# Optimization experiments

Hardware: AMD Instinct MI355X
Metric: run time of the kernel (lower is better)

Reference implementation:

```python
import jax, jax.numpy as jnp
import numpy as np

B, S, D = 4, 2048, 1024
H = 16
DH = D // H  # dim_q = dim_k = 64
F = 4096
EPS = 1e-5


def setup_inputs() -> dict:
    key = jax.random.key(0)
    ks = jax.random.split(key, 16)
    sd = 0.02
    inp = {
        'x': jax.random.normal(ks[0], (B, S, D), jnp.float32),
        'wq': jax.random.normal(ks[1], (H, D, DH), jnp.float32) * sd,
        'bq': jnp.zeros((H, DH), jnp.float32),
        'wk': jax.random.normal(ks[2], (H, D, DH), jnp.float32) * sd,
        'bk': jnp.zeros((H, DH), jnp.float32),
        'wv': jax.random.normal(ks[3], (H, D, DH), jnp.float32) * sd,
        'bv': jnp.zeros((H, DH), jnp.float32),
        'wo': jax.random.normal(ks[4], (H * DH, D), jnp.float32) * sd,
        'bo': jnp.zeros((D,), jnp.float32),
        'ln1_g': jnp.ones((D,), jnp.float32),
        'ln1_b': jnp.zeros((D,), jnp.float32),
        'w1': jax.random.normal(ks[5], (D, F), jnp.float32) * sd,
        'b1': jnp.zeros((F,), jnp.float32),
        'w2': jax.random.normal(ks[6], (F, D), jnp.float32) * sd,
        'b2': jnp.zeros((D,), jnp.float32),
        'ln2_g': jnp.ones((D,), jnp.float32),
        'ln2_b': jnp.zeros((D,), jnp.float32),
    }
    return inp


def _layernorm(x, g, b):
    mu = jnp.mean(x, axis=-1, keepdims=True)
    var = jnp.mean(jnp.square(x - mu), axis=-1, keepdims=True)
    return (x - mu) * jax.lax.rsqrt(var + EPS) * g + b


def _encoder_layer(x, wq, bq, wk, bk, wv, bv, wo, bo, ln1_g, ln1_b,
                   w1, b1, w2, b2, ln2_g, ln2_b):
    # Multi-head attention (all heads batched via einsum)
    q = jnp.einsum('bsd,hde->bhse', x, wq) + bq[:, None, :]
    k = jnp.einsum('bsd,hde->bhse', x, wk) + bk[:, None, :]
    v = jnp.einsum('bsd,hde->bhse', x, wv) + bv[:, None, :]
    scores = jnp.einsum('bhqe,bhke->bhqk', q, k) / jnp.sqrt(jnp.float32(DH))
    p = jax.nn.softmax(scores, axis=-1)
    o = jnp.einsum('bhqk,bhke->bhqe', p, v)  # [B,H,S,DH]
    o = o.transpose(0, 2, 1, 3).reshape(B, S, H * DH)  # concat heads
    attn = o @ wo + bo
    y = _layernorm(x + attn, ln1_g, ln1_b)  # post-norm residual
    # Feed-forward
    ff = jax.nn.relu(y @ w1 + b1) @ w2 + b2
    return _layernorm(y + ff, ln2_g, ln2_b)


def reference(x, wq, bq, wk, bk, wv, bv, wo, bo, ln1_g, ln1_b,
              w1, b1, w2, b2, ln2_g, ln2_b):
    return _encoder_layer(x, wq, bq, wk, bk, wv, bv, wo, bo, ln1_g, ln1_b,
                          w1, b1, w2, b2, ln2_g, ln2_b)
```

## Files before the change

kernel.cpp:

```cpp
#include <hip/hip_runtime.h>
#include <stdint.h>


typedef short bf16x8 __attribute__((ext_vector_type(8)));
typedef unsigned short u16x8 __attribute__((ext_vector_type(8)));
typedef float f32x4 __attribute__((ext_vector_type(4)));
typedef unsigned int u32x2 __attribute__((ext_vector_type(2)));

#define MFMA16(a, b, c) __builtin_amdgcn_mfma_f32_16x16x32_bf16((a), (b), (c), 0, 0, 0)

#define QSCALE 0.1803368801111204f

__device__ __forceinline__ float b2f(unsigned short u) {
    union { unsigned u32; float f; } x;
    x.u32 = ((unsigned)u) << 16;
    return x.f;
}
__device__ __forceinline__ unsigned short f2b(float f) {
    union { float f; unsigned u; } x;
    x.f = f;
    unsigned r = x.u + 0x7fff + ((x.u >> 16) & 1);
    return (unsigned short)(r >> 16);
}

__device__ __forceinline__ void gl16(const unsigned short* g, unsigned short* l) {
    __builtin_amdgcn_global_load_lds(
        (__attribute__((address_space(1))) unsigned int*)(unsigned long)g,
        (__attribute__((address_space(3))) unsigned int*)l, 16, 0, 0);
}

__global__ __launch_bounds__(256) void f2b_bulk(const float* __restrict__ in,
                                                unsigned short* __restrict__ out) {
    const long i = ((long)blockIdx.x * 256 + threadIdx.x) * 8;
    float4 a = *(const float4*)&in[i];
    float4 b = *(const float4*)&in[i + 4];
    u16x8 u;
    u[0] = f2b(a.x); u[1] = f2b(a.y); u[2] = f2b(a.z); u[3] = f2b(a.w);
    u[4] = f2b(b.x); u[5] = f2b(b.y); u[6] = f2b(b.z); u[7] = f2b(b.w);
    *(u16x8*)&out[i] = u;
}

__global__ void transpose_f2b(const float* __restrict__ in,
                              unsigned short* __restrict__ out,
                              int R, int C, long in_batch_stride,
                              int out_row0, int out_ld) {
    __shared__ float tile[32][33];
    const int batch = blockIdx.z;
    const float* src = in + (long)batch * in_batch_stride;
    const int c0 = blockIdx.x * 32, r0 = blockIdx.y * 32;
    const int tx = threadIdx.x, ty = threadIdx.y;
#pragma unroll
    for (int i = 0; i < 32; i += 8)
        tile[ty + i][tx] = src[(long)(r0 + ty + i) * C + c0 + tx];
    __syncthreads();
#pragma unroll
    for (int i = 0; i < 32; i += 8)
        out[(long)(out_row0 + batch * C + c0 + ty + i) * out_ld + r0 + tx] =
            f2b(tile[tx][ty + i]);
}

__global__ void transpose_v(const unsigned short* __restrict__ qkv,
                            unsigned short* __restrict__ vt) {
    __shared__ unsigned short tile[32][33];
    const int bh = blockIdx.z;
    const int b = bh >> 4, h = bh & 15;
    const int s0 = blockIdx.x * 32, e0 = blockIdx.y * 32;
    const int tx = threadIdx.x, ty = threadIdx.y;
    const unsigned short* src = qkv + ((long)b * 2048) * 3072 + 2048 + h * 64;
#pragma unroll
    for (int i = 0; i < 32; i += 8)
        tile[ty + i][tx] = src[(long)(s0 + ty + i) * 3072 + e0 + tx];
    __syncthreads();
    unsigned short* dst = vt + ((long)bh * 64) * 2048;
#pragma unroll
    for (int i = 0; i < 32; i += 8)
        dst[(long)(e0 + ty + i) * 2048 + s0 + tx] = tile[tx][ty + i];
}

__global__ void concat_bias(const float* __restrict__ bq,
                            const float* __restrict__ bk,
                            const float* __restrict__ bv,
                            float* __restrict__ out) {
    int n = blockIdx.x * 256 + threadIdx.x;
    out[n] = (n < 1024) ? bq[n] : (n < 2048) ? bk[n - 1024] : bv[n - 2048];
}

__device__ __forceinline__ float to_f(float v) { return v; }
__device__ __forceinline__ float to_f(unsigned short v) { return b2f(v); }

template <typename RT>
__global__ __launch_bounds__(512, 2) void gemm256(
    const unsigned short* __restrict__ A, const unsigned short* __restrict__ Bt,
    unsigned short* __restrict__ C, const float* __restrict__ bias,
    const RT* __restrict__ resid, int M, int N, int K, int op) {
    __shared__ __align__(16) unsigned short As[4][256 * 32];
    __shared__ __align__(16) unsigned short Bs[4][256 * 32];
    const int tid = threadIdx.x;
    const int lane = tid & 63;
    const int wave = tid >> 6;
    const int quad = lane >> 4, lr = lane & 15;
    const int wr = wave >> 2, wc = wave & 3;

    const int nx = gridDim.x;
    const int nwg = nx * gridDim.y;
    const int orig = blockIdx.y * nx + blockIdx.x;
    const int wg = (orig & 7) * (nwg >> 3) + (orig >> 3);
    const long n0 = (long)(wg % nx) * 256;
    const long m0 = (long)(wg / nx) * 256;

    f32x4 acc[8][4] = {};

    const int trow = tid >> 2;
    const int tch = ((tid & 3) ^ ((tid >> 3) & 3)) * 8;
    const unsigned short* gA0 = A + (m0 + trow) * (long)K + tch;
    const unsigned short* gA1 = A + (m0 + 128 + trow) * (long)K + tch;
    const unsigned short* gB0 = Bt + (n0 + trow) * (long)K + tch;
    const unsigned short* gB1 = Bt + (n0 + 128 + trow) * (long)K + tch;
    unsigned short* const dA = &As[0][0] + tid * 8;
    unsigned short* const dB = &Bs[0][0] + tid * 8;

    int aoff[8], boff[4];
#pragma unroll
    for (int mi = 0; mi < 8; mi++) {
        const int r = wr * 128 + mi * 16 + lr;
        aoff[mi] = r * 32 + (quad ^ ((r >> 1) & 3)) * 8;
    }
#pragma unroll
    for (int ni = 0; ni < 4; ni++) {
        const int r = wc * 64 + ni * 16 + lr;
        boff[ni] = r * 32 + (quad ^ ((r >> 1) & 3)) * 8;
    }

#define STAGE_A(si)                                                   \
    {                                                                 \
        gl16(gA0 + (long)(si) * 32, dA + ((si) & 3) * 8192);          \
        gl16(gA1 + (long)(si) * 32, dA + ((si) & 3) * 8192 + 4096);   \
    }
#define STAGE_B(si)                                                   \
    {                                                                 \
        gl16(gB0 + (long)(si) * 32, dB + ((si) & 3) * 8192);          \
        gl16(gB1 + (long)(si) * 32, dB + ((si) & 3) * 8192 + 4096);   \
    }

    const int S = K >> 5;
    for (int s = 0; s < 3; s++) {
        STAGE_A(s);
        STAGE_B(s);
    }
    asm volatile("s_waitcnt vmcnt(8)" ::: "memory");
    __builtin_amdgcn_s_barrier();

    for (int s = 0; s < S; ++s) {
        const int slot = s & 3;
        const unsigned short* as_ = &As[slot][0];
        const unsigned short* bs_ = &Bs[slot][0];
        const bool st = (s + 3) < S;
        bf16x8 af[8], bf[4];
#pragma unroll
        for (int mi = 0; mi < 8; mi++) af[mi] = *(const bf16x8*)&as_[aoff[mi]];
        bf[0] = *(const bf16x8*)&bs_[boff[0]];
        bf[1] = *(const bf16x8*)&bs_[boff[1]];
        if (st) STAGE_A(s + 3);
        __builtin_amdgcn_s_barrier();
        asm volatile("s_waitcnt lgkmcnt(0)" ::: "memory");
        __builtin_amdgcn_sched_barrier(0);
        __builtin_amdgcn_s_setprio(1);
#pragma unroll
        for (int mi = 0; mi < 8; mi++) {
            acc[mi][0] = MFMA16(af[mi], bf[0], acc[mi][0]);
            acc[mi][1] = MFMA16(af[mi], bf[1], acc[mi][1]);
        }
        __builtin_amdgcn_s_setprio(0);
        __builtin_amdgcn_s_barrier();
        __builtin_amdgcn_sched_barrier(0);
        bf[2] = *(const bf16x8*)&bs_[boff[2]];
        bf[3] = *(const bf16x8*)&bs_[boff[3]];
        if (st) STAGE_B(s + 3);
        __builtin_amdgcn_s_barrier();
        asm volatile("s_waitcnt lgkmcnt(0)" ::: "memory");
        __builtin_amdgcn_sched_barrier(0);
        __builtin_amdgcn_s_setprio(1);
#pragma unroll
        for (int mi = 0; mi < 8; mi++) {
            acc[mi][2] = MFMA16(af[mi], bf[2], acc[mi][2]);
            acc[mi][3] = MFMA16(af[mi], bf[3], acc[mi][3]);
        }
        __builtin_amdgcn_s_setprio(0);
        if (s + 3 < S) {
            asm volatile("s_waitcnt vmcnt(8)" ::: "memory");
        } else if (s + 2 < S) {
            asm volatile("s_waitcnt vmcnt(4)" ::: "memory");
        } else {
            asm volatile("s_waitcnt vmcnt(0)" ::: "memory");
        }
        __builtin_amdgcn_s_barrier();
        __builtin_amdgcn_sched_barrier(0);
    }
#undef STAGE_A
#undef STAGE_B

#pragma unroll
    for (int ni = 0; ni < 4; ni++) {
        const long col = n0 + wc * 64 + ni * 16 + lr;
        const float bv = bias ? bias[col] : 0.0f;
        const float cscale = (op == 2 && col < 1024) ? QSCALE : 1.0f;
#pragma unroll
        for (int mi = 0; mi < 8; mi++) {
#pragma unroll
            for (int r = 0; r < 4; r++) {
                const long row = m0 + wr * 128 + mi * 16 + quad * 4 + r;
                float v = (acc[mi][ni][r] + bv) * cscale;
                if (resid) v += to_f(resid[row * (long)N + col]);
                if (op == 1) v = fmaxf(v, 0.0f);
                C[row * (long)N + col] = f2b(v);
            }
        }
    }
}

template <int TAG, typename RT>
__global__ __launch_bounds__(512, 2) void gemmK64(
    const unsigned short* __restrict__ A, const unsigned short* __restrict__ Bt,
    unsigned short* __restrict__ C, const float* __restrict__ bias,
    const RT* __restrict__ resid, int M, int N, int K, int op) {
    __shared__ __align__(16) unsigned short As[3][256 * 64];
    __shared__ __align__(16) unsigned short Bs[3][128 * 64];
    const int tid = threadIdx.x;
    const int lane = tid & 63;
    const int wave = tid >> 6;
    const int quad = lane >> 4, lr = lane & 15;
    const int wr = wave >> 1, wc = wave & 1;

    const int nx = gridDim.x;
    const int nwg = nx * gridDim.y;
    const int orig = blockIdx.y * nx + blockIdx.x;
    const int wg = (orig & 7) * (nwg >> 3) + (orig >> 3);
    const long n0 = (long)(wg % nx) * 128;
    const long m0 = (long)(wg / nx) * 256;

    f32x4 acc[4][4] = {};

    const int trow = tid >> 3;
    const int tch = ((tid & 7) ^ ((tid >> 4) & 7)) * 8;
    const unsigned short* gA = A + (m0 + trow) * (long)K + tch;
    const unsigned short* gB = Bt + (n0 + trow) * (long)K + tch;
    const long rs64 = 64 * (long)K;
    unsigned short* const dA = &As[0][0] + tid * 8;
    unsigned short* const dB = &Bs[0][0] + tid * 8;

    int aoff[2][4], boff[2][4];
#pragma unroll
    for (int kc = 0; kc < 2; kc++) {
#pragma unroll
        for (int mi = 0; mi < 4; mi++) {
            const int r = wr * 64 + mi * 16 + lr;
            aoff[kc][mi] = r * 64 + (((kc << 2) | quad) ^ ((r >> 1) & 7)) * 8;
        }
#pragma unroll
        for (int ni = 0; ni < 4; ni++) {
            const int r = wc * 64 + ni * 16 + lr;
            boff[kc][ni] = r * 64 + (((kc << 2) | quad) ^ ((r >> 1) & 7)) * 8;
        }
    }

#define KSTAGE_H1(si)                                                   \
    {                                                                   \
        const long _kk = (long)(si) * 64;                               \
        const int _sl = (si) % 3;                                       \
        gl16(gA + _kk, dA + _sl * 16384);                               \
        gl16(gA + rs64 + _kk, dA + _sl * 16384 + 4096);                 \
        gl16(gB + _kk, dB + _sl * 8192);                                \
    }
#define KSTAGE_H2(si)                                                   \
    {                                                                   \
        const long _kk = (long)(si) * 64;                               \
        const int _sl = (si) % 3;                                       \
        gl16(gA + 2 * rs64 + _kk, dA + _sl * 16384 + 8192);             \
        gl16(gA + 3 * rs64 + _kk, dA + _sl * 16384 + 12288);            \
        gl16(gB + rs64 + _kk, dB + _sl * 8192 + 4096);                  \
    }

    const int S = K >> 6;
    KSTAGE_H1(0);
    KSTAGE_H2(0);
    KSTAGE_H1(1);
    KSTAGE_H2(1);
    asm volatile("s_waitcnt vmcnt(6)" ::: "memory");
    __builtin_amdgcn_s_barrier();

    for (int s = 0; s < S; ++s) {
        const int sl = s % 3;
        const unsigned short* as_ = &As[sl][0];
        const unsigned short* bs_ = &Bs[sl][0];
        const bool st = (s + 2) < S;
        bf16x8 a0[4], b0[4], a1[4], b1[4];
#pragma unroll
        for (int mi = 0; mi < 4; mi++) a0[mi] = *(const bf16x8*)&as_[aoff[0][mi]];
#pragma unroll
        for (int ni = 0; ni < 4; ni++) b0[ni] = *(const bf16x8*)&bs_[boff[0][ni]];
        if (st) KSTAGE_H1(s + 2);
        __builtin_amdgcn_s_barrier();
        asm volatile("s_waitcnt lgkmcnt(0)" ::: "memory");
        __builtin_amdgcn_sched_barrier(0);
        __builtin_amdgcn_s_setprio(1);
#pragma unroll
        for (int mi = 0; mi < 4; mi++)
#pragma unroll
            for (int ni = 0; ni < 4; ni++)
                acc[mi][ni] = MFMA16(a0[mi], b0[ni], acc[mi][ni]);
        __builtin_amdgcn_s_setprio(0);
        __builtin_amdgcn_s_barrier();
        __builtin_amdgcn_sched_barrier(0);
#pragma unroll
        for (int mi = 0; mi < 4; mi++) a1[mi] = *(const bf16x8*)&as_[aoff[1][mi]];
#pragma unroll
        for (int ni = 0; ni < 4; ni++) b1[ni] = *(const bf16x8*)&bs_[boff[1][ni]];
        if (st) KSTAGE_H2(s + 2);
        __builtin_amdgcn_s_barrier();
        asm volatile("s_waitcnt lgkmcnt(0)" ::: "memory");
        __builtin_amdgcn_sched_barrier(0);
        __builtin_amdgcn_s_setprio(1);
#pragma unroll
        for (int mi = 0; mi < 4; mi++)
#pragma unroll
            for (int ni = 0; ni < 4; ni++)
                acc[mi][ni] = MFMA16(a1[mi], b1[ni], acc[mi][ni]);
        __builtin_amdgcn_s_setprio(0);
        if (st) {
            asm volatile("s_waitcnt vmcnt(6)" ::: "memory");
        } else {
            asm volatile("s_waitcnt vmcnt(0)" ::: "memory");
        }
        __builtin_amdgcn_s_barrier();
        __builtin_amdgcn_sched_barrier(0);
    }
#undef KSTAGE_H1
#undef KSTAGE_H2

#pragma unroll
    for (int ni = 0; ni < 4; ni++) {
        const long col = n0 + wc * 64 + ni * 16 + lr;
        const float bv = bias ? bias[col] : 0.0f;
        const float cscale = (op == 2 && col < 1024) ? QSCALE : 1.0f;
#pragma unroll
        for (int mi = 0; mi < 4; mi++) {
#pragma unroll
            for (int r = 0; r < 4; r++) {
                const long row = m0 + wr * 64 + mi * 16 + quad * 4 + r;
                float v = (acc[mi][ni][r] + bv) * cscale;
                if (resid) v += to_f(resid[row * (long)N + col]);
                if (op == 1) v = fmaxf(v, 0.0f);
                C[row * (long)N + col] = f2b(v);
            }
        }
    }
}

__global__ __launch_bounds__(256, 5) void attn_kernel(
    const unsigned short* __restrict__ qkv, const unsigned short* __restrict__ vt,
    unsigned short* __restrict__ o) {
    __shared__ __align__(16) unsigned short Klds[2][64 * 64];
    __shared__ __align__(16) unsigned short Vlds[2][64 * 64];
    const int l = blockIdx.x;
    const int bh = ((l >> 8) << 3) | (l & 7);
    const int qt = (l >> 3) & 31;
    const int b = bh >> 4, h = bh & 15;
    const int tid = threadIdx.x;
    const int wave = tid >> 6, lane = tid & 63;
    const int quad = lane >> 4, lr = lane & 15;
    const long rowbase = (long)b * 2048;
    const int qb = qt * 64 + wave * 16;

    bf16x8 q0, q1;
    {
        const unsigned short* qrow = qkv + (rowbase + qb + lr) * 3072 + h * 64;
        q0 = *(const bf16x8*)&qrow[quad * 8];
        q1 = *(const bf16x8*)&qrow[32 + quad * 8];
    }

    bf16x8 ones;
#pragma unroll
    for (int i = 0; i < 8; i++) ones[i] = (short)0x3F80;

    const int srow = lane >> 3;
    const int sxc = (lane & 7) ^ srow;
    const unsigned short* kp =
        qkv + (rowbase + wave * 16 + srow) * 3072 + 1024 + h * 64 + sxc * 8;
    const unsigned short* vp =
        vt + ((long)bh * 64 + wave * 16 + srow) * 2048 + sxc * 8;
    const long KADV = 64L * 3072;
    unsigned short* const kd0 = &Klds[0][wave * 16 * 64];
    unsigned short* const vd0 = &Vlds[0][wave * 16 * 64];

#define STAGE(bf)                                                     \
    {                                                                 \
        gl16(kp, kd0 + (bf)*4096);                                    \
        gl16(kp + 8 * 3072, kd0 + (bf)*4096 + 8 * 64);                \
        gl16(vp, vd0 + (bf)*4096);                                    \
        gl16(vp + 8 * 2048, vd0 + (bf)*4096 + 8 * 64);                \
    }

    f32x4 oacc[4] = {};
    f32x4 dacc = {};

    const int x7 = lr & 7;
    const int c00 = (quad ^ x7) * 8;
    const int c01 = ((4 | quad) ^ x7) * 8;

    STAGE(0);
    __syncthreads();

    for (int kt = 0; kt < 32; kt++) {
        const int buf = kt & 1;
        if (kt < 31) {
            kp += KADV;
            vp += 64;
            STAGE(buf ^ 1);
        }
        const unsigned short* kb = &Klds[buf][0];
        f32x4 s4[4];
#pragma unroll
        for (int nt = 0; nt < 4; nt++) {
            const unsigned short* krow = kb + (nt * 16 + lr) * 64;
            bf16x8 k0 = *(const bf16x8*)&krow[c00];
            bf16x8 k1 = *(const bf16x8*)&krow[c01];
            f32x4 z = {};
            z = MFMA16(k0, q0, z);
            z = MFMA16(k1, q1, z);
            s4[nt] = z;
        }
        unsigned pwv[4][2];
#pragma unroll
        for (int nt = 0; nt < 4; nt++) {
            float p0 = exp2f(s4[nt][0]);
            float p1 = exp2f(s4[nt][1]);
            float p2 = exp2f(s4[nt][2]);
            float p3 = exp2f(s4[nt][3]);
            asm("v_cvt_pk_bf16_f32 %0, %1, %2"
                : "=v"(pwv[nt][0]) : "v"(p0), "v"(p1));
            asm("v_cvt_pk_bf16_f32 %0, %1, %2"
                : "=v"(pwv[nt][1]) : "v"(p2), "v"(p3));
        }
        unsigned pq[2][4];
#pragma unroll
        for (int kc = 0; kc < 2; kc++)
#pragma unroll
            for (int tl = 0; tl < 2; tl++) {
                u32x2 y = __builtin_amdgcn_permlane32_swap(
                    pwv[2 * kc][tl], pwv[2 * kc + 1][tl], false, false);
                u32x2 z = __builtin_amdgcn_permlane16_swap(y[0], y[1], false, false);
                pq[kc][tl] = z[0];
                pq[kc][2 + tl] = z[1];
            }

        const unsigned short* vb = &Vlds[buf][0];
#pragma unroll
        for (int kc = 0; kc < 2; kc++) {
            union { unsigned u[4]; bf16x8 h; } pu;
            pu.u[0] = pq[kc][0]; pu.u[1] = pq[kc][1];
            pu.u[2] = pq[kc][2]; pu.u[3] = pq[kc][3];
            const int vc = kc ? c01 : c00;
            dacc = MFMA16(ones, pu.h, dacc);
#pragma unroll
            for (int nt = 0; nt < 4; nt++) {
                bf16x8 va = *(const bf16x8*)&vb[(nt * 16 + lr) * 64 + vc];
                oacc[nt] = MFMA16(va, pu.h, oacc[nt]);
            }
        }
        __syncthreads();
    }

    const float rinv = 1.0f / dacc[0];

    const long orow = rowbase + qb + lr;
#pragma unroll
    for (int nt = 0; nt < 4; nt++) {
        ushort4 ov = {f2b(oacc[nt][0] * rinv), f2b(oacc[nt][1] * rinv),
                      f2b(oacc[nt][2] * rinv), f2b(oacc[nt][3] * rinv)};
        *(ushort4*)&o[orow * 1024 + h * 64 + nt * 16 + quad * 4] = ov;
    }
#undef STAGE
}

__device__ __forceinline__ void st4(float* p, float a, float b, float c, float d) {
    float4 v = {a, b, c, d};
    *(float4*)p = v;
}
__device__ __forceinline__ void st4(unsigned short* p, float a, float b, float c,
                                    float d) {
    ushort4 v = {f2b(a), f2b(b), f2b(c), f2b(d)};
    *(ushort4*)p = v;
}

template <typename OT>
__global__ __launch_bounds__(256) void ln_kernel(
    const unsigned short* __restrict__ in, const float* __restrict__ g,
    const float* __restrict__ b, OT* __restrict__ out) {
    __shared__ float red[4];
    const long row = blockIdx.x;
    const int tid = threadIdx.x;
    ushort4 u = *(const ushort4*)&in[row * 1024 + tid * 4];
    float v[4] = {b2f(u.x), b2f(u.y), b2f(u.z), b2f(u.w)};
    float s = v[0] + v[1] + v[2] + v[3];
#pragma unroll
    for (int off = 32; off > 0; off >>= 1) s += __shfl_down(s, off, 64);
    if ((tid & 63) == 0) red[tid >> 6] = s;
    __syncthreads();
    const float mu = (red[0] + red[1] + red[2] + red[3]) * (1.0f / 1024.0f);
    __syncthreads();
    float d[4], sq = 0.f;
#pragma unroll
    for (int i = 0; i < 4; i++) { d[i] = v[i] - mu; sq += d[i] * d[i]; }
#pragma unroll
    for (int off = 32; off > 0; off >>= 1) sq += __shfl_down(sq, off, 64);
    if ((tid & 63) == 0) red[tid >> 6] = sq;
    __syncthreads();
    const float var = (red[0] + red[1] + red[2] + red[3]) * (1.0f / 1024.0f);
    const float rs = rsqrtf(var + 1e-5f);
    float4 gu = *(const float4*)&g[tid * 4];
    float4 bu = *(const float4*)&b[tid * 4];
    st4(&out[row * 1024 + tid * 4], d[0] * rs * gu.x + bu.x,
        d[1] * rs * gu.y + bu.y, d[2] * rs * gu.z + bu.z,
        d[3] * rs * gu.w + bu.w);
}

extern "C" void kernel_launch(void* const* d_in, const int* in_sizes, int n_in,
                              void* d_out, int out_size, void* d_ws, size_t ws_size,
                              hipStream_t stream) {
    (void)in_sizes; (void)n_in; (void)out_size; (void)ws_size;
    const float* x   = (const float*)d_in[0];
    const float* wq  = (const float*)d_in[1];
    const float* bq  = (const float*)d_in[2];
    const float* wk  = (const float*)d_in[3];
    const float* bk  = (const float*)d_in[4];
    const float* wv  = (const float*)d_in[5];
    const float* bv  = (const float*)d_in[6];
    const float* wo  = (const float*)d_in[7];
    const float* bo  = (const float*)d_in[8];
    const float* g1  = (const float*)d_in[9];
    const float* be1 = (const float*)d_in[10];
    const float* w1  = (const float*)d_in[11];
    const float* b1  = (const float*)d_in[12];
    const float* w2  = (const float*)d_in[13];
    const float* b2  = (const float*)d_in[14];
    const float* g2  = (const float*)d_in[15];
    const float* be2 = (const float*)d_in[16];

    char* ws = (char*)d_ws;
    const size_t MB = 1024 * 1024;
    unsigned short* WT_QKV = (unsigned short*)(ws + 0);
    unsigned short* WT_O   = (unsigned short*)(ws + 6 * MB);
    unsigned short* WT_1   = (unsigned short*)(ws + 8 * MB);
    unsigned short* WT_2   = (unsigned short*)(ws + 16 * MB);
    float*          BQKV   = (float*)(ws + 24 * MB);
    unsigned short* XB     = (unsigned short*)(ws + 25 * MB);
    unsigned short* QKV    = (unsigned short*)(ws + 41 * MB);
    unsigned short* O      = (unsigned short*)(ws + 89 * MB);
    unsigned short* R1     = (unsigned short*)(ws + 25 * MB);
    unsigned short* Y      = (unsigned short*)(ws + 41 * MB);
    unsigned short* R2     = (unsigned short*)(ws + 57 * MB);
    unsigned short* Hb     = (unsigned short*)(ws + 73 * MB);
    unsigned short* VT     = (unsigned short*)(ws + 137 * MB);
    float*          OUT    = (float*)d_out;

    const dim3 tb(32, 8, 1);
    transpose_f2b<<<dim3(2, 32, 16), tb, 0, stream>>>(wq, WT_QKV, 1024, 64, 65536L, 0, 1024);
    transpose_f2b<<<dim3(2, 32, 16), tb, 0, stream>>>(wk, WT_QKV, 1024, 64, 65536L, 1024, 1024);
    transpose_f2b<<<dim3(2, 32, 16), tb, 0, stream>>>(wv, WT_QKV, 1024, 64, 65536L, 2048, 1024);
    transpose_f2b<<<dim3(32, 32, 1), tb, 0, stream>>>(wo, WT_O, 1024, 1024, 0L, 0, 1024);
    transpose_f2b<<<dim3(128, 32, 1), tb, 0, stream>>>(w1, WT_1, 1024, 4096, 0L, 0, 1024);
    transpose_f2b<<<dim3(32, 128, 1), tb, 0, stream>>>(w2, WT_2, 4096, 1024, 0L, 0, 4096);
    concat_bias<<<dim3(12), 256, 0, stream>>>(bq, bk, bv, BQKV);
    f2b_bulk<<<dim3(4096), 256, 0, stream>>>(x, XB);

    gemmK64<0, unsigned short><<<dim3(24, 32), 512, 0, stream>>>(
        XB, WT_QKV, QKV, BQKV, (const unsigned short*)nullptr, 8192, 3072, 1024, 2);
    transpose_v<<<dim3(64, 2, 64), tb, 0, stream>>>(QKV, VT);
    attn_kernel<<<dim3(2048), 256, 0, stream>>>(QKV, VT, O);
    gemmK64<1, float><<<dim3(8, 32), 512, 0, stream>>>(
        O, WT_O, R1, bo, x, 8192, 1024, 1024, 0);
    ln_kernel<unsigned short><<<dim3(8192), 256, 0, stream>>>(R1, g1, be1, Y);
    gemm256<unsigned short><<<dim3(16, 32), 512, 0, stream>>>(
        Y, WT_1, Hb, b1, (const unsigned short*)nullptr, 8192, 4096, 1024, 1);
    gemmK64<2, unsigned short><<<dim3(8, 32), 512, 0, stream>>>(
        Hb, WT_2, R2, b2, Y, 8192, 1024, 4096, 0);
    ln_kernel<float><<<dim3(8192), 256, 0, stream>>>(R2, g2, be2, OUT);
}
```

Measured before the change: 579.7 us.

## Triple-buffer K/V tiles in attention with partial vmcnt waits

```diff
diff --git a/kernel.cpp b/kernel.cpp
--- a/kernel.cpp
+++ b/kernel.cpp
@@ -356,11 +356,11 @@
     }
 }
 
-__global__ __launch_bounds__(256, 5) void attn_kernel(
+__global__ __launch_bounds__(256, 3) void attn_kernel(
     const unsigned short* __restrict__ qkv, const unsigned short* __restrict__ vt,
     unsigned short* __restrict__ o) {
-    __shared__ __align__(16) unsigned short Klds[2][64 * 64];
-    __shared__ __align__(16) unsigned short Vlds[2][64 * 64];
+    __shared__ __align__(16) unsigned short Klds[3][64 * 64];
+    __shared__ __align__(16) unsigned short Vlds[3][64 * 64];
     const int l = blockIdx.x;
     const int bh = ((l >> 8) << 3) | (l & 7);
     const int qt = (l >> 3) & 31;
@@ -392,12 +392,14 @@
     unsigned short* const kd0 = &Klds[0][wave * 16 * 64];
     unsigned short* const vd0 = &Vlds[0][wave * 16 * 64];
 
-#define STAGE(bf)                                                     \
+#define STAGE(sl)                                                     \
     {                                                                 \
-        gl16(kp, kd0 + (bf)*4096);                                    \
-        gl16(kp + 8 * 3072, kd0 + (bf)*4096 + 8 * 64);                \
-        gl16(vp, vd0 + (bf)*4096);                                    \
-        gl16(vp + 8 * 2048, vd0 + (bf)*4096 + 8 * 64);                \
+        gl16(kp, kd0 + (sl)*4096);                                    \
+        gl16(kp + 8 * 3072, kd0 + (sl)*4096 + 8 * 64);                \
+        gl16(vp, vd0 + (sl)*4096);                                    \
+        gl16(vp + 8 * 2048, vd0 + (sl)*4096 + 8 * 64);                \
+        kp += KADV;                                                   \
+        vp += 64;                                                     \
     }
 
     f32x4 oacc[4] = {};
@@ -408,16 +410,14 @@
     const int c01 = ((4 | quad) ^ x7) * 8;
 
     STAGE(0);
-    __syncthreads();
+    STAGE(1);
+    asm volatile("s_waitcnt vmcnt(4)" ::: "memory");
+    __builtin_amdgcn_s_barrier();
 
     for (int kt = 0; kt < 32; kt++) {
-        const int buf = kt & 1;
-        if (kt < 31) {
-            kp += KADV;
-            vp += 64;
-            STAGE(buf ^ 1);
-        }
-        const unsigned short* kb = &Klds[buf][0];
+        const int sl = kt % 3;
+        if (kt < 30) STAGE((kt + 2) % 3);
+        const unsigned short* kb = &Klds[sl][0];
         f32x4 s4[4];
 #pragma unroll
         for (int nt = 0; nt < 4; nt++) {
@@ -453,7 +453,7 @@
                 pq[kc][2 + tl] = z[1];
             }
 
-        const unsigned short* vb = &Vlds[buf][0];
+        const unsigned short* vb = &Vlds[sl][0];
 #pragma unroll
         for (int kc = 0; kc < 2; kc++) {
             union { unsigned u[4]; bf16x8 h; } pu;
@@ -467,7 +467,13 @@
                 oacc[nt] = MFMA16(va, pu.h, oacc[nt]);
             }
         }
-        __syncthreads();
+        if (kt < 30) {
+            asm volatile("s_waitcnt vmcnt(4)" ::: "memory");
+            __builtin_amdgcn_s_barrier();
+        } else if (kt == 30) {
+            asm volatile("s_waitcnt vmcnt(0)" ::: "memory");
+            __builtin_amdgcn_s_barrier();
+        }
     }
 
     const float rinv = 1.0f / dacc[0];
```

New measurement: 589.6 us. No clear change (+1.7%).
